# Performance work log

Measured on AMD Instinct MI355X. Metric: run time of the kernel, lower is better.

Reference implementation:

```python
import jax, jax.numpy as jnp
import numpy as np

DIM = 1024
Q_HEADS = 16
KV_HEADS = 4
DIM_HEAD = DIM // Q_HEADS  # 64
SOFTCLAMP = 50.0
EPS = 1e-8


def rotate_half(x):
    x_even = x[..., ::2]
    x_odd = x[..., 1::2]
    return jnp.stack([-x_odd, x_even], axis=-1).reshape(x.shape)


def setup_inputs() -> dict:
    key = jax.random.key(0)
    ks = jax.random.split(key, 10)
    B, S = 1, 2048
    dim_q = DIM_HEAD * Q_HEADS   # 1024
    dim_kv = DIM_HEAD * KV_HEADS  # 256
    std = 0.02
    x = jax.random.normal(ks[0], (B, S, DIM), dtype=jnp.float32)
    positions = jnp.broadcast_to(jnp.arange(S, dtype=jnp.int32)[None, :], (B, S))
    # causal mask: True = disallowed (torch semantics: allowed = ~attn_mask)
    attn_mask = jnp.triu(jnp.ones((S, S), dtype=bool), k=1)
    return {
        "x": x,
        "positions": positions,
        "attn_mask": attn_mask,
        "Wq": jax.random.normal(ks[1], (DIM, dim_q), jnp.float32) * std,
        "Wk": jax.random.normal(ks[2], (DIM, dim_kv), jnp.float32) * std,
        "Wv": jax.random.normal(ks[3], (DIM, dim_kv), jnp.float32) * std,
        "Wo": jax.random.normal(ks[4], (dim_q, DIM), jnp.float32) * std,
        "Wg": jax.random.normal(ks[5], (DIM, Q_HEADS), jnp.float32) * std,
        "Wm": jax.random.normal(ks[6], (DIM, KV_HEADS), jnp.float32) * std,
        "bm": jnp.zeros((KV_HEADS,), jnp.float32),
        "Wvr": jax.random.normal(ks[7], (DIM, dim_kv), jnp.float32) * std,
        "k_scale": jnp.ones((KV_HEADS, DIM_HEAD), jnp.float32),
    }


def reference(x, positions, attn_mask, Wq, Wk, Wv, Wo, Wg, Wm, bm, Wvr, k_scale):
    b, s, _ = x.shape
    h, qh, dh = KV_HEADS, Q_HEADS, DIM_HEAD
    g = qh // h

    q = (x @ Wq).reshape(b, s, qh, dh).transpose(0, 2, 1, 3)  # [b,qh,s,dh]
    k = (x @ Wk).reshape(b, s, h, dh).transpose(0, 2, 1, 3)   # [b,h,s,dh]
    v = (x @ Wv).reshape(b, s, h, dh).transpose(0, 2, 1, 3)

    # value-residual gating: v = lerp(v, residual_v, mix)
    residual_v = (x @ Wvr).reshape(b, s, h, dh).transpose(0, 2, 1, 3)
    mix = jax.nn.sigmoid(x @ Wm + bm).transpose(0, 2, 1)[..., None]  # [b,h,s,1]
    v = v + mix * (residual_v - v)

    # multi-head RMSNorm on k
    rms = jnp.sqrt(jnp.mean(k * k, axis=-1, keepdims=True) + EPS)
    k = k / rms * k_scale[None, :, None, :]

    # rotary embeddings (identical for all heads -> broadcast over head dim)
    inv_freq = 1.0 / (10000.0 ** (jnp.arange(0, dh, 2, dtype=jnp.float32) / dh))
    freqs = positions.astype(jnp.float32)[..., None] * inv_freq  # [b,s,dh/2]
    cos = jnp.repeat(jnp.cos(freqs), 2, axis=-1)[:, None, :, :]  # [b,1,s,dh]
    sin = jnp.repeat(jnp.sin(freqs), 2, axis=-1)[:, None, :, :]
    q = q * cos + rotate_half(q) * sin
    k = k * cos + rotate_half(k) * sin

    # grouped-query attention with softclamped scores
    scale = dh ** -0.5
    qg = q.reshape(b, h, g, s, dh)
    sim = jnp.einsum('bhgqd,bhkd->bhgqk', qg, k) * scale
    sim = jnp.tanh(sim / SOFTCLAMP) * SOFTCLAMP
    allowed = ~attn_mask  # [s,s]
    sim = jnp.where(allowed[None, None, None, :, :], sim, jnp.finfo(sim.dtype).min)
    attn = jax.nn.softmax(sim, axis=-1)
    out = jnp.einsum('bhgqk,bhkd->bhgqd', attn, v).reshape(b, qh, s, dh)

    # per-query-head sigmoid gates
    gates = jax.nn.sigmoid(x @ Wg).transpose(0, 2, 1)[..., None]  # [b,qh,s,1]
    out = out * gates

    out = out.transpose(0, 2, 1, 3).reshape(b, s, qh * dh)
    return out @ Wo
```

## Files before the change

kernel.cpp:

```cpp
#include <hip/hip_runtime.h>
#include <hip/hip_bf16.h>
#include <math.h>

typedef unsigned short u16;
typedef unsigned int u32;
typedef __attribute__((ext_vector_type(8))) __bf16 bf16x8;
typedef __attribute__((ext_vector_type(4))) float f32x4;

__device__ inline u16 f2bf(float f) {
  u32 b = __float_as_uint(f);
  b += 0x7FFFu + ((b >> 16) & 1u);
  return (u16)(b >> 16);
}
__device__ inline float bf2f(u16 b) { return __uint_as_float((u32)b << 16); }

__device__ __forceinline__ void gll16(const void* gp, void* lp) {
  __builtin_amdgcn_global_load_lds(
      (const __attribute__((address_space(1))) void*)gp,
      (__attribute__((address_space(3))) void*)lp, 16, 0, 0);
}

__global__ __launch_bounds__(256) void prep_all_k(
    const float* __restrict__ x, const int* __restrict__ positions,
    const float* __restrict__ Wq, const float* __restrict__ Wk,
    const float* __restrict__ Wv, const float* __restrict__ Wvr,
    const float* __restrict__ Wo, const float* __restrict__ Wg,
    const float* __restrict__ Wm, u16* __restrict__ xb,
    u16* __restrict__ WallT, u16* __restrict__ WoT, float* __restrict__ rtab) {
  __shared__ float tile[32][33];
  int bid = blockIdx.x, tid = threadIdx.x;
  if (bid < 1024) {
    int i = (bid * 256 + tid) * 8;
    float4 v0 = *(const float4*)&x[i];
    float4 v1 = *(const float4*)&x[i + 4];
    uint4 pk;
    pk.x = (u32)f2bf(v0.x) | ((u32)f2bf(v0.y) << 16);
    pk.y = (u32)f2bf(v0.z) | ((u32)f2bf(v0.w) << 16);
    pk.z = (u32)f2bf(v1.x) | ((u32)f2bf(v1.y) << 16);
    pk.w = (u32)f2bf(v1.z) | ((u32)f2bf(v1.w) << 16);
    *(uint4*)&xb[i] = pk;
    return;
  }
  if (bid >= 3968) {
    int idx = (bid - 3968) * 256 + tid;
    int s = idx >> 5, f = idx & 31;
    float inv = __expf(-(float)f * (9.210340371976184f / 32.f));
    float ang = (float)positions[s] * inv;
    rtab[(size_t)s * 64 + f] = cosf(ang);
    rtab[(size_t)s * 64 + 32 + f] = sinf(ang);
    return;
  }
  int b2 = bid - 1024;
  int k0 = (b2 & 31) * 32;
  int ybl = b2 >> 5;
  int tx = tid & 31, ty = tid >> 5;
  const float* src;
  int scol, sN, drow;
  u16* dst;
  if (ybl >= 60) {
    src = Wo; scol = (ybl - 60) * 32; sN = 1024; dst = WoT; drow = scol;
  } else {
    int n0 = ybl * 32;
    if (n0 >= 1792) {
#pragma unroll
      for (int j = 0; j < 4; ++j) {
        int n = n0 + ty * 4 + j, j2 = n - 1792, k = k0 + tx;
        float val = (j2 < 16) ? Wg[(size_t)k * 16 + j2]
                  : (j2 < 20) ? Wm[(size_t)k * 4 + (j2 - 16)] : 0.f;
        WallT[(size_t)n * 1024 + k] = f2bf(val);
      }
      return;
    }
    dst = WallT; drow = n0;
    if (n0 < 1024) { src = Wq; scol = n0; sN = 1024; }
    else if (n0 < 1280) { src = Wk; scol = n0 - 1024; sN = 256; }
    else if (n0 < 1536) { src = Wv; scol = n0 - 1280; sN = 256; }
    else { src = Wvr; scol = n0 - 1536; sN = 256; }
  }
#pragma unroll
  for (int j = 0; j < 4; ++j)
    tile[ty * 4 + j][tx] = src[(size_t)(k0 + ty * 4 + j) * sN + scol + tx];
  __syncthreads();
#pragma unroll
  for (int j = 0; j < 4; ++j)
    dst[(size_t)(drow + ty * 4 + j) * 1024 + k0 + tx] = f2bf(tile[tx][ty * 4 + j]);
}

template <int BM, bool BF16_OUT>
__global__ __launch_bounds__(512) void gemm_bf16_k(
    const u16* __restrict__ A, const u16* __restrict__ Bt, void* __restrict__ Cv,
    int M, int N, int K) {
  constexpr int MI = BM / 32;
  __shared__ __align__(16) u16 As[2][BM * 64];
  __shared__ __align__(16) u16 Bs[2][128 * 64];
  int tid = threadIdx.x;
  int w = tid >> 6, l = tid & 63;
  int wr = w >> 2, wc = w & 3;
  int lr = l & 15, lg = l >> 4;
  int lrow = l >> 3, lcol = (l & 7) * 8;
  int m0 = blockIdx.y * BM, n0 = blockIdx.x * 128;
  f32x4 zero = {0.f, 0.f, 0.f, 0.f};
  f32x4 acc[MI][2];
#pragma unroll
  for (int mi = 0; mi < MI; ++mi)
#pragma unroll
    for (int ni = 0; ni < 2; ++ni) acc[mi][ni] = zero;

  auto gstage = [&](int buf, int kt) {
#pragma unroll
    for (int ts = 0; ts < BM / 64; ++ts) {
      int seg = ts * 8 + w;
      gll16(&A[(size_t)(m0 + seg * 8 + lrow) * K + kt + lcol],
            &As[buf][seg * 512]);
    }
#pragma unroll
    for (int ts = 0; ts < 2; ++ts) {
      int seg = ts * 8 + w;
      gll16(&Bt[(size_t)(n0 + seg * 8 + lrow) * K + kt + lcol],
            &Bs[buf][seg * 512]);
    }
  };

  gstage(0, 0);
  __syncthreads();
  int nt = K >> 6;
#pragma unroll 1
  for (int t = 0; t < nt; ++t) {
    int cur = t & 1;
    if (t + 1 < nt) gstage(cur ^ 1, (t + 1) * 64);
#pragma unroll
    for (int kw = 0; kw < 2; ++kw) {
      bf16x8 af[MI], bfr[2];
#pragma unroll
      for (int mi = 0; mi < MI; ++mi)
        af[mi] = *(const bf16x8*)&As[cur][(wr * (BM / 2) + mi * 16 + lr) * 64 + kw * 32 + lg * 8];
#pragma unroll
      for (int ni = 0; ni < 2; ++ni)
        bfr[ni] = *(const bf16x8*)&Bs[cur][(wc * 32 + ni * 16 + lr) * 64 + kw * 32 + lg * 8];
#pragma unroll
      for (int mi = 0; mi < MI; ++mi)
#pragma unroll
        for (int ni = 0; ni < 2; ++ni)
          acc[mi][ni] = __builtin_amdgcn_mfma_f32_16x16x32_bf16(
              af[mi], bfr[ni], acc[mi][ni], 0, 0, 0);
    }
    __syncthreads();
  }
#pragma unroll
  for (int mi = 0; mi < MI; ++mi)
#pragma unroll
    for (int ni = 0; ni < 2; ++ni)
#pragma unroll
      for (int r = 0; r < 4; ++r) {
        int row = m0 + wr * (BM / 2) + mi * 16 + lg * 4 + r;
        int col = n0 + wc * 32 + ni * 16 + lr;
        if (BF16_OUT)
          ((u16*)Cv)[(size_t)row * N + col] = f2bf(acc[mi][ni][r]);
        else
          ((float*)Cv)[(size_t)row * N + col] = acc[mi][ni][r];
      }
}

#define TPAD 66
__global__ __launch_bounds__(256) void postv_k(
    const float* __restrict__ bm, const float* __restrict__ ksc,
    const float* __restrict__ rtab, const u16* __restrict__ qkvrb,
    u16* __restrict__ kb, u16* __restrict__ vtb, float* __restrict__ g_out) {
  __shared__ u16 tile[64 * TPAD];
  int s0 = blockIdx.x * 64, h = blockIdx.y;
  int t = threadIdx.x;
  int sl = t >> 2, db = (t & 3) * 16;
  int s = s0 + sl;
  const u16* row = qkvrb + (size_t)s * 1920;
  if (h == 0) {
#pragma unroll
    for (int j = 0; j < 4; ++j) {
      int idx = j * 256 + t;
      int sg = s0 + (idx >> 4), hh = idx & 15;
      g_out[sg * 16 + hh] =
          1.f / (1.f + __expf(-bf2f(qkvrb[(size_t)sg * 1920 + 1792 + hh])));
    }
  }
  float kvv[16];
  float ssq = 0.f;
  {
    uint4 kr0 = *(const uint4*)&row[1024 + h * 64 + db];
    uint4 kr1 = *(const uint4*)&row[1024 + h * 64 + db + 8];
    const u16* p0 = (const u16*)&kr0;
    const u16* p1 = (const u16*)&kr1;
#pragma unroll
    for (int j = 0; j < 8; ++j) {
      kvv[j] = bf2f(p0[j]);
      ssq += kvv[j] * kvv[j];
    }
#pragma unroll
    for (int j = 0; j < 8; ++j) {
      kvv[8 + j] = bf2f(p1[j]);
      ssq += kvv[8 + j] * kvv[8 + j];
    }
  }
  ssq += __shfl_xor(ssq, 1);
  ssq += __shfl_xor(ssq, 2);
  float rinv = 1.f / sqrtf(ssq * (1.f / 64.f) + 1e-8f);
  const float* tr = rtab + (size_t)s * 64;
  float cs[8], sn[8];
  *(float4*)cs = *(const float4*)&tr[db >> 1];
  *(float4*)(cs + 4) = *(const float4*)&tr[(db >> 1) + 4];
  *(float4*)sn = *(const float4*)&tr[32 + (db >> 1)];
  *(float4*)(sn + 4) = *(const float4*)&tr[32 + (db >> 1) + 4];
  float scl[16];
  *(float4*)scl = *(const float4*)&ksc[h * 64 + db];
  *(float4*)(scl + 4) = *(const float4*)&ksc[h * 64 + db + 4];
  *(float4*)(scl + 8) = *(const float4*)&ksc[h * 64 + db + 8];
  *(float4*)(scl + 12) = *(const float4*)&ksc[h * 64 + db + 12];
  {
    u16 outk[16];
#pragma unroll
    for (int j = 0; j < 8; ++j) {
      float e = kvv[2 * j] * rinv * scl[2 * j];
      float o = kvv[2 * j + 1] * rinv * scl[2 * j + 1];
      outk[2 * j] = f2bf(e * cs[j] - o * sn[j]);
      outk[2 * j + 1] = f2bf(o * cs[j] + e * sn[j]);
    }
    u16* kdst = kb + ((size_t)h * 2048 + s) * 64 + db;
    *(uint4*)kdst = *(uint4*)outk;
    *(uint4*)(kdst + 8) = *(uint4*)(outk + 8);
  }
  {
    float mixv = 1.f / (1.f + __expf(-(bf2f(row[1808 + h]) + bm[h])));
    uint4 vr0 = *(const uint4*)&row[1280 + h * 64 + db];
    uint4 vr1 = *(const uint4*)&row[1280 + h * 64 + db + 8];
    uint4 rr0 = *(const uint4*)&row[1536 + h * 64 + db];
    uint4 rr1 = *(const uint4*)&row[1536 + h * 64 + db + 8];
    const u16* vp0 = (const u16*)&vr0;
    const u16* vp1 = (const u16*)&vr1;
    const u16* rp0 = (const u16*)&rr0;
    const u16* rp1 = (const u16*)&rr1;
#pragma unroll
    for (int j = 0; j < 8; ++j) {
      float vv = bf2f(vp0[j]);
      tile[sl * TPAD + db + j] = f2bf(vv + mixv * (bf2f(rp0[j]) - vv));
    }
#pragma unroll
    for (int j = 0; j < 8; ++j) {
      float vv = bf2f(vp1[j]);
      tile[sl * TPAD + db + 8 + j] = f2bf(vv + mixv * (bf2f(rp1[j]) - vv));
    }
  }
  __syncthreads();
  {
    int d = t >> 2, sb = (t & 3) * 16;
    u16 vals[16];
#pragma unroll
    for (int j = 0; j < 16; ++j) vals[j] = tile[(sb + j) * TPAD + d];
    uint4 a, b;
    a.x = (u32)vals[0] | ((u32)vals[1] << 16);
    a.y = (u32)vals[2] | ((u32)vals[3] << 16);
    a.z = (u32)vals[4] | ((u32)vals[5] << 16);
    a.w = (u32)vals[6] | ((u32)vals[7] << 16);
    b.x = (u32)vals[8] | ((u32)vals[9] << 16);
    b.y = (u32)vals[10] | ((u32)vals[11] << 16);
    b.z = (u32)vals[12] | ((u32)vals[13] << 16);
    b.w = (u32)vals[14] | ((u32)vals[15] << 16);
    u16* dst = vtb + ((size_t)h * 64 + d) * 2048 + s0 + sb;
    *(uint4*)dst = a;
    *(uint4*)(dst + 8) = b;
  }
}

__global__ __launch_bounds__(512) void attn_k(
    const u16* __restrict__ qkvrb, const u16* __restrict__ kb,
    const u16* __restrict__ vtb, const float* __restrict__ g,
    const float* __restrict__ rtab, u16* __restrict__ aob) {
  __shared__ __align__(16) u16 smem[57344];
  int head = blockIdx.x, hkv = head >> 2;
  int tid = threadIdx.x;
  int w = tid >> 6, l = tid & 63;
  int grp = w >> 2, wi = w & 3;
  int lr = l & 15, lg = l >> 4;
  int gtid = wi * 64 + l;
  u16* KsBase = smem + grp * 24576;
  u32* pw = (u32*)(smem + 49152) + (size_t)w * 512;
  float* mbuf = (float*)smem;
  f32x4 zero = {0.f, 0.f, 0.f, 0.f};
  const float L2E = 1.4426950408889634f;
  const float NB = -72.13475204444817f;
  int sw = (lr & 7) << 2;
  int u0 = ((lg ^ (lr & 7)) << 3);
  int srow = l >> 3;
  int sunit = (l & 7) ^ srow;
  const u16* ksrc = kb + ((size_t)hkv * 2048 + srow) * 64 + sunit * 8;
  const u16* vsrc = vtb + ((size_t)(hkv * 64 + srow)) * 2048 + sunit * 8;
  auto stageChunk = [&](int b, int cc) {
    u16* Kb = KsBase + b * 8192;
#pragma unroll
    for (int t = 0; t < 2; ++t) {
      int seg = wi * 2 + t;
      gll16(ksrc + (size_t)(cc * 64 + seg * 8) * 64, Kb + seg * 512);
      gll16(vsrc + (size_t)(seg * 8) * 2048 + cc * 64, Kb + 4096 + seg * 512);
    }
  };
#pragma unroll 1
  for (int half = 0; half < 2; ++half) {
    int rb = half ? (int)blockIdx.y : (31 - (int)blockIdx.y);
    int row0 = rb * 64;
    int qglob = row0 + wi * 16 + lr;
    const u16* qrow = qkvrb + (size_t)qglob * 1920 + head * 64;
    const float* trq = rtab + (size_t)qglob * 64;
    bf16x8 qf0, qf1;
    {
      float ce0[4], se0[4], ce1[4], se1[4];
      *(float4*)ce0 = *(const float4*)&trq[lg * 4];
      *(float4*)se0 = *(const float4*)&trq[32 + lg * 4];
      *(float4*)ce1 = *(const float4*)&trq[16 + lg * 4];
      *(float4*)se1 = *(const float4*)&trq[48 + lg * 4];
      uint4 qr0 = *(const uint4*)&qrow[lg * 8];
      uint4 qr1 = *(const uint4*)&qrow[32 + lg * 8];
      const u16* qp0 = (const u16*)&qr0;
      const u16* qp1 = (const u16*)&qr1;
      union { u32 w[4]; bf16x8 v; } b0, b1;
#pragma unroll
      for (int j = 0; j < 4; ++j) {
        float e0 = bf2f(qp0[2 * j]), e1 = bf2f(qp0[2 * j + 1]);
        float r0 = (e0 * ce0[j] - e1 * se0[j]) * 0.125f;
        float r1 = (e1 * ce0[j] + e0 * se0[j]) * 0.125f;
        b0.w[j] = (u32)f2bf(r0) | ((u32)f2bf(r1) << 16);
        float f0 = bf2f(qp1[2 * j]), f1 = bf2f(qp1[2 * j + 1]);
        float t0 = (f0 * ce1[j] - f1 * se1[j]) * 0.125f;
        float t1 = (f1 * ce1[j] + f0 * se1[j]) * 0.125f;
        b1.w[j] = (u32)f2bf(t0) | ((u32)f2bf(t1) << 16);
      }
      qf0 = b0.v;
      qf1 = b1.v;
    }
    f32x4 acc_o[4];
#pragma unroll
    for (int nd = 0; nd < 4; ++nd) acc_o[nd] = zero;
    float l_part = 0.f;
    int c = grp;
    if (c <= rb) stageChunk(0, c);
    if (c + 2 <= rb) {
      stageChunk(1, c + 2);
      asm volatile("s_waitcnt vmcnt(4)\n\ts_barrier" ::: "memory");
    } else {
      asm volatile("s_waitcnt vmcnt(0)\n\ts_barrier" ::: "memory");
    }
    int nmax = (rb >> 1) + 1;
    int bufc = 0;
#pragma unroll 1
    for (int i = 0; i < nmax; ++i, c += 2) {
      bool valid = (c <= rb);
      bool sn = (c + 4 <= rb);
      if (sn) {
        int bufs = bufc - 1;
        if (bufs < 0) bufs = 2;
        stageChunk(bufs, c + 4);
      }
      if (valid) {
        u16* Ks = KsBase + bufc * 8192;
        u16* Vt = Ks + 4096;
        int kbase = c * 64;
        __builtin_amdgcn_s_setprio(1);
        f32x4 sa[4];
#pragma unroll
        for (int ni = 0; ni < 4; ++ni) {
          const u16* kp = &Ks[(ni * 16 + lr) * 64];
          bf16x8 a0 = *(const bf16x8*)&kp[u0];
          bf16x8 a1 = *(const bf16x8*)&kp[u0 ^ 32];
          f32x4 t = __builtin_amdgcn_mfma_f32_16x16x32_bf16(a0, qf0, zero, 0, 0, 0);
          sa[ni] = __builtin_amdgcn_mfma_f32_16x16x32_bf16(a1, qf1, t, 0, 0, 0);
        }
        bool diag = (c == rb);
#pragma unroll
        for (int ni = 0; ni < 4; ++ni) {
          float pv[4];
#pragma unroll
          for (int r = 0; r < 4; ++r) {
            float sv = fminf(fmaxf(sa[ni][r], -60.f), 60.f);
            float t2 = sv * 0.02f;
            float u = t2 * t2;
            float cl = sv * fmaf(u, fmaf(u, 0.13333333f, -0.33333333f), 1.f);
            float p = __builtin_amdgcn_exp2f(fmaf(cl, L2E, NB));
            if (diag && (kbase + ni * 16 + lg * 4 + r) > qglob) p = 0.f;
            pv[r] = p;
            l_part += p;
          }
          u32 w0, w1;
          asm("v_cvt_pk_bf16_f32 %0, %1, %2" : "=v"(w0) : "v"(pv[0]), "v"(pv[1]));
          asm("v_cvt_pk_bf16_f32 %0, %1, %2" : "=v"(w1) : "v"(pv[2]), "v"(pv[3]));
          uint2 pr;
          pr.x = w0;
          pr.y = w1;
          *(uint2*)&pw[lr * 32 + ((ni * 8 + lg * 2) ^ sw)] = pr;
        }
        bf16x8 pfa = *(const bf16x8*)&pw[lr * 32 + ((lg * 4) ^ sw)];
        bf16x8 pfb = *(const bf16x8*)&pw[lr * 32 + ((16 + lg * 4) ^ sw)];
#pragma unroll
        for (int nd = 0; nd < 4; ++nd) {
          const u16* vp = &Vt[(nd * 16 + lr) * 64];
          bf16x8 v0 = *(const bf16x8*)&vp[u0];
          bf16x8 v1 = *(const bf16x8*)&vp[u0 ^ 32];
          acc_o[nd] = __builtin_amdgcn_mfma_f32_16x16x32_bf16(pfa, v0, acc_o[nd], 0, 0, 0);
          acc_o[nd] = __builtin_amdgcn_mfma_f32_16x16x32_bf16(pfb, v1, acc_o[nd], 0, 0, 0);
        }
        __builtin_amdgcn_s_setprio(0);
      }
      if (sn) {
        asm volatile("s_waitcnt vmcnt(4)\n\ts_barrier" ::: "memory");
      } else {
        asm volatile("s_waitcnt vmcnt(0)\n\ts_barrier" ::: "memory");
      }
      bufc = (bufc == 2) ? 0 : bufc + 1;
    }
    l_part += __shfl_xor(l_part, 16);
    l_part += __shfl_xor(l_part, 32);
    if (grp == 1) {
      float* mb = mbuf + (size_t)gtid * 17;
#pragma unroll
      for (int nd = 0; nd < 4; ++nd)
#pragma unroll
        for (int r = 0; r < 4; ++r) mb[nd * 4 + r] = acc_o[nd][r];
      mb[16] = l_part;
    }
    __syncthreads();
    if (grp == 0) {
      const float* mb = mbuf + (size_t)gtid * 17;
      float lt = l_part + mb[16];
#pragma unroll
      for (int r = 0; r < 4; ++r) {
        int row = row0 + wi * 16 + lg * 4 + r;
        float lv = __shfl(lt, lg * 4 + r);
        float sc = g[row * 16 + head] * __builtin_amdgcn_rcpf(lv);
#pragma unroll
        for (int nd = 0; nd < 4; ++nd)
          aob[(size_t)row * 1024 + head * 64 + nd * 16 + lr] =
              f2bf((acc_o[nd][r] + mb[nd * 4 + r]) * sc);
      }
    }
    __syncthreads();
  }
}

extern "C" void kernel_launch(void* const* d_in, const int* in_sizes, int n_in,
                              void* d_out, int out_size, void* d_ws,
                              size_t ws_size, hipStream_t stream) {
  const float* x = (const float*)d_in[0];
  const int* positions = (const int*)d_in[1];
  const float* Wq = (const float*)d_in[3];
  const float* Wk = (const float*)d_in[4];
  const float* Wv = (const float*)d_in[5];
  const float* Wo = (const float*)d_in[6];
  const float* Wg = (const float*)d_in[7];
  const float* Wm = (const float*)d_in[8];
  const float* bm = (const float*)d_in[9];
  const float* Wvr = (const float*)d_in[10];
  const float* ksc = (const float*)d_in[11];
  float* out = (float*)d_out;

  u16* xb = (u16*)d_ws;
  u16* WallT = xb + (size_t)2048 * 1024;
  u16* WoT = WallT + (size_t)1920 * 1024;
  u16* qkvrb = WoT + (size_t)1024 * 1024;
  u16* kbuf = qkvrb + (size_t)2048 * 1920;
  u16* vtb = kbuf + (size_t)4 * 2048 * 64;
  float* gbuf = (float*)(vtb + (size_t)4 * 2048 * 64);
  float* rtab = gbuf + (size_t)2048 * 16;
  u16* aob = xb;

  prep_all_k<<<4224, 256, 0, stream>>>(x, positions, Wq, Wk, Wv, Wvr, Wo, Wg,
                                       Wm, xb, WallT, WoT, rtab);
  gemm_bf16_k<128, true><<<dim3(15, 16), 512, 0, stream>>>(xb, WallT, qkvrb,
                                                           2048, 1920, 1024);
  postv_k<<<dim3(32, 4), 256, 0, stream>>>(bm, ksc, rtab, qkvrb, kbuf, vtb,
                                           gbuf);
  attn_k<<<dim3(16, 16), 512, 0, stream>>>(qkvrb, kbuf, vtb, gbuf, rtab, aob);
  gemm_bf16_k<64, false><<<dim3(8, 32), 512, 0, stream>>>(aob, WoT, out, 2048,
                                                          1024, 1024);
}
```

Baseline: 88.38 us.

## Stage K/V in chunk pairs with double buffering to halve barriers

The attention kernel's K/V staging moves from a triple-buffered single-chunk pipeline to a double-buffered scheme. Each stage loads two 64-key chunks per group. Each loop iteration now processes two chunks between barriers, so barrier and waitcnt overhead per chunk drops. In exchange, LDS use grows from about 112KB to 144KB. Every iteration also issues loads, including clamped redundant loads past the diagonal, and the full vmcnt(0) sync removes some of the finer-grained load overlap.

```diff
diff --git a/kernel.cpp b/kernel.cpp
--- a/kernel.cpp
+++ b/kernel.cpp
@@ -272,15 +272,15 @@
     const u16* __restrict__ qkvrb, const u16* __restrict__ kb,
     const u16* __restrict__ vtb, const float* __restrict__ g,
     const float* __restrict__ rtab, u16* __restrict__ aob) {
-  __shared__ __align__(16) u16 smem[57344];
+  __shared__ __align__(16) u16 smem[73728];
   int head = blockIdx.x, hkv = head >> 2;
   int tid = threadIdx.x;
   int w = tid >> 6, l = tid & 63;
   int grp = w >> 2, wi = w & 3;
   int lr = l & 15, lg = l >> 4;
   int gtid = wi * 64 + l;
-  u16* KsBase = smem + grp * 24576;
-  u32* pw = (u32*)(smem + 49152) + (size_t)w * 512;
+  u16* GrpBase = smem + grp * 32768;
+  u32* pw = (u32*)(smem + 65536) + (size_t)w * 512;
   float* mbuf = (float*)smem;
   f32x4 zero = {0.f, 0.f, 0.f, 0.f};
   const float L2E = 1.4426950408889634f;
@@ -291,15 +291,6 @@
   int sunit = (l & 7) ^ srow;
   const u16* ksrc = kb + ((size_t)hkv * 2048 + srow) * 64 + sunit * 8;
   const u16* vsrc = vtb + ((size_t)(hkv * 64 + srow)) * 2048 + sunit * 8;
-  auto stageChunk = [&](int b, int cc) {
-    u16* Kb = KsBase + b * 8192;
-#pragma unroll
-    for (int t = 0; t < 2; ++t) {
-      int seg = wi * 2 + t;
-      gll16(ksrc + (size_t)(cc * 64 + seg * 8) * 64, Kb + seg * 512);
-      gll16(vsrc + (size_t)(seg * 8) * 2048 + cc * 64, Kb + 4096 + seg * 512);
-    }
-  };
 #pragma unroll 1
   for (int half = 0; half < 2; ++half) {
     int rb = half ? (int)blockIdx.y : (31 - (int)blockIdx.y);
@@ -337,80 +328,82 @@
 #pragma unroll
     for (int nd = 0; nd < 4; ++nd) acc_o[nd] = zero;
     float l_part = 0.f;
-    int c = grp;
-    if (c <= rb) stageChunk(0, c);
-    if (c + 2 <= rb) {
-      stageChunk(1, c + 2);
-      asm volatile("s_waitcnt vmcnt(4)\n\ts_barrier" ::: "memory");
-    } else {
-      asm volatile("s_waitcnt vmcnt(0)\n\ts_barrier" ::: "memory");
-    }
-    int nmax = (rb >> 1) + 1;
-    int bufc = 0;
+    auto stagePair = [&](int slot, int c0) {
+      u16* S = GrpBase + slot * 16384;
+      int cA = c0 <= rb ? c0 : rb;
+      int cB = c0 + 1 <= rb ? c0 + 1 : rb;
+#pragma unroll
+      for (int t = 0; t < 2; ++t) {
+        int seg = wi * 2 + t;
+        gll16(ksrc + (size_t)(cA * 64 + seg * 8) * 64, S + seg * 512);
+        gll16(vsrc + (size_t)(seg * 8) * 2048 + cA * 64, S + 4096 + seg * 512);
+        gll16(ksrc + (size_t)(cB * 64 + seg * 8) * 64, S + 8192 + seg * 512);
+        gll16(vsrc + (size_t)(seg * 8) * 2048 + cB * 64,
+              S + 12288 + seg * 512);
+      }
+    };
+    int c = grp * 2;
+    stagePair(0, c);
+    __syncthreads();
+    int nmax = (rb >> 2) + 1;
 #pragma unroll 1
-    for (int i = 0; i < nmax; ++i, c += 2) {
-      bool valid = (c <= rb);
-      bool sn = (c + 4 <= rb);
-      if (sn) {
-        int bufs = bufc - 1;
-        if (bufs < 0) bufs = 2;
-        stageChunk(bufs, c + 4);
-      }
-      if (valid) {
-        u16* Ks = KsBase + bufc * 8192;
-        u16* Vt = Ks + 4096;
-        int kbase = c * 64;
-        __builtin_amdgcn_s_setprio(1);
-        f32x4 sa[4];
-#pragma unroll
-        for (int ni = 0; ni < 4; ++ni) {
-          const u16* kp = &Ks[(ni * 16 + lr) * 64];
-          bf16x8 a0 = *(const bf16x8*)&kp[u0];
-          bf16x8 a1 = *(const bf16x8*)&kp[u0 ^ 32];
-          f32x4 t = __builtin_amdgcn_mfma_f32_16x16x32_bf16(a0, qf0, zero, 0, 0, 0);
-          sa[ni] = __builtin_amdgcn_mfma_f32_16x16x32_bf16(a1, qf1, t, 0, 0, 0);
+    for (int i = 0; i < nmax; ++i, c += 4) {
+      stagePair((i + 1) & 1, c + 4);
+      u16* slotBase = GrpBase + (i & 1) * 16384;
+      __builtin_amdgcn_s_setprio(1);
+#pragma unroll
+      for (int h = 0; h < 2; ++h) {
+        int ch = c + h;
+        if (ch <= rb) {
+          u16* Ks = slotBase + h * 8192;
+          u16* Vt = Ks + 4096;
+          int kbase = ch * 64;
+          f32x4 sa[4];
+#pragma unroll
+          for (int ni = 0; ni < 4; ++ni) {
+            const u16* kp = &Ks[(ni * 16 + lr) * 64];
+            bf16x8 a0 = *(const bf16x8*)&kp[u0];
+            bf16x8 a1 = *(const bf16x8*)&kp[u0 ^ 32];
+            f32x4 t = __builtin_amdgcn_mfma_f32_16x16x32_bf16(a0, qf0, zero, 0, 0, 0);
+            sa[ni] = __builtin_amdgcn_mfma_f32_16x16x32_bf16(a1, qf1, t, 0, 0, 0);
+          }
+          bool diag = (ch == rb);
+#pragma unroll
+          for (int ni = 0; ni < 4; ++ni) {
+            float pv[4];
+#pragma unroll
+            for (int r = 0; r < 4; ++r) {
+              float sv = fminf(fmaxf(sa[ni][r], -60.f), 60.f);
+              float t2 = sv * 0.02f;
+              float u = t2 * t2;
+              float cl = sv * fmaf(u, fmaf(u, 0.13333333f, -0.33333333f), 1.f);
+              float p = __builtin_amdgcn_exp2f(fmaf(cl, L2E, NB));
+              if (diag && (kbase + ni * 16 + lg * 4 + r) > qglob) p = 0.f;
+              pv[r] = p;
+              l_part += p;
+            }
+            u32 w0, w1;
+            asm("v_cvt_pk_bf16_f32 %0, %1, %2" : "=v"(w0) : "v"(pv[0]), "v"(pv[1]));
+            asm("v_cvt_pk_bf16_f32 %0, %1, %2" : "=v"(w1) : "v"(pv[2]), "v"(pv[3]));
+            uint2 pr;
+            pr.x = w0;
+            pr.y = w1;
+            *(uint2*)&pw[lr * 32 + ((ni * 8 + lg * 2) ^ sw)] = pr;
+          }
+          bf16x8 pfa = *(const bf16x8*)&pw[lr * 32 + ((lg * 4) ^ sw)];
+          bf16x8 pfb = *(const bf16x8*)&pw[lr * 32 + ((16 + lg * 4) ^ sw)];
+#pragma unroll
+          for (int nd = 0; nd < 4; ++nd) {
+            const u16* vp = &Vt[(nd * 16 + lr) * 64];
+            bf16x8 v0 = *(const bf16x8*)&vp[u0];
+            bf16x8 v1 = *(const bf16x8*)&vp[u0 ^ 32];
+            acc_o[nd] = __builtin_amdgcn_mfma_f32_16x16x32_bf16(pfa, v0, acc_o[nd], 0, 0, 0);
+            acc_o[nd] = __builtin_amdgcn_mfma_f32_16x16x32_bf16(pfb, v1, acc_o[nd], 0, 0, 0);
+          }
         }
-        bool diag = (c == rb);
-#pragma unroll
-        for (int ni = 0; ni < 4; ++ni) {
-          float pv[4];
-#pragma unroll
-          for (int r = 0; r < 4; ++r) {
-            float sv = fminf(fmaxf(sa[ni][r], -60.f), 60.f);
-            float t2 = sv * 0.02f;
-            float u = t2 * t2;
-            float cl = sv * fmaf(u, fmaf(u, 0.13333333f, -0.33333333f), 1.f);
-            float p = __builtin_amdgcn_exp2f(fmaf(cl, L2E, NB));
-            if (diag && (kbase + ni * 16 + lg * 4 + r) > qglob) p = 0.f;
-            pv[r] = p;
-            l_part += p;
-          }
-          u32 w0, w1;
-          asm("v_cvt_pk_bf16_f32 %0, %1, %2" : "=v"(w0) : "v"(pv[0]), "v"(pv[1]));
-          asm("v_cvt_pk_bf16_f32 %0, %1, %2" : "=v"(w1) : "v"(pv[2]), "v"(pv[3]));
-          uint2 pr;
-          pr.x = w0;
-          pr.y = w1;
-          *(uint2*)&pw[lr * 32 + ((ni * 8 + lg * 2) ^ sw)] = pr;
-        }
-        bf16x8 pfa = *(const bf16x8*)&pw[lr * 32 + ((lg * 4) ^ sw)];
-        bf16x8 pfb = *(const bf16x8*)&pw[lr * 32 + ((16 + lg * 4) ^ sw)];
-#pragma unroll
-        for (int nd = 0; nd < 4; ++nd) {
-          const u16* vp = &Vt[(nd * 16 + lr) * 64];
-          bf16x8 v0 = *(const bf16x8*)&vp[u0];
-          bf16x8 v1 = *(const bf16x8*)&vp[u0 ^ 32];
-          acc_o[nd] = __builtin_amdgcn_mfma_f32_16x16x32_bf16(pfa, v0, acc_o[nd], 0, 0, 0);
-          acc_o[nd] = __builtin_amdgcn_mfma_f32_16x16x32_bf16(pfb, v1, acc_o[nd], 0, 0, 0);
-        }
-        __builtin_amdgcn_s_setprio(0);
-      }
-      if (sn) {
-        asm volatile("s_waitcnt vmcnt(4)\n\ts_barrier" ::: "memory");
-      } else {
-        asm volatile("s_waitcnt vmcnt(0)\n\ts_barrier" ::: "memory");
-      }
-      bufc = (bufc == 2) ? 0 : bufc + 1;
+      }
+      __builtin_amdgcn_s_setprio(0);
+      __syncthreads();
     }
     l_part += __shfl_xor(l_part, 16);
     l_part += __shfl_xor(l_part, 32);
```

Result: no change. 87.61 us (-0.9%).
